# Optimization experiments

Measured on AMD Instinct MI355X. Metric: run time of the kernel, lower is better.

Reference implementation:

```python
import jax, jax.numpy as jnp
import numpy as np

N_NODES = 100000
N_EDGES = 1600000
N_ROOTS = 2048


def _with_self_loops(edge_index, num_nodes):
    loop = jnp.arange(num_nodes, dtype=edge_index.dtype)
    src = jnp.concatenate([edge_index[0], loop])
    dst = jnp.concatenate([edge_index[1], loop])
    return src, dst


def gcn_conv(x, w, b, src, dst, num_nodes):
    xw = x @ w  # [N, Fout]
    deg = jax.ops.segment_sum(jnp.ones_like(dst, dtype=xw.dtype), dst,
                              num_segments=num_nodes)
    dinv = jnp.where(deg > 0, jax.lax.rsqrt(jnp.maximum(deg, 1.0)) * (deg > 0), 0.0)
    dinv = jnp.where(deg > 0, deg ** -0.5, 0.0)
    norm = dinv[src] * dinv[dst]  # [E+N]
    msgs = norm[:, None] * xw[src]  # [E+N, Fout] -- dominant memory traffic
    out = jax.ops.segment_sum(msgs, dst, num_segments=num_nodes)
    return out + b


def setup_inputs() -> dict:
    key = jax.random.key(0)
    ks = jax.random.split(key, 10)
    x = jax.random.normal(ks[0], (N_NODES, 256), dtype=jnp.float32)
    edge_index = jax.random.randint(ks[1], (2, N_EDGES), 0, N_NODES, dtype=jnp.int32)
    bu_edge_index = jax.random.randint(ks[2], (2, N_EDGES), 0, N_NODES, dtype=jnp.int32)
    rootindex = jax.random.randint(ks[3], (N_ROOTS,), 0, N_NODES, dtype=jnp.int32)
    def glorot(k, shape):
        lim = (6.0 / (shape[0] + shape[1])) ** 0.5
        return jax.random.uniform(k, shape, jnp.float32, -lim, lim)
    return {
        "x": x, "edge_index": edge_index, "bu_edge_index": bu_edge_index,
        "rootindex": rootindex,
        "w1": glorot(ks[4], (256, 128)), "b1": jnp.zeros((128,), jnp.float32),
        "w2": glorot(ks[5], (128, 128)), "b2": jnp.zeros((128,), jnp.float32),
        "w3": glorot(ks[6], (256, 128)), "b3": jnp.zeros((128,), jnp.float32),
        "w4": glorot(ks[7], (128, 128)), "b4": jnp.zeros((128,), jnp.float32),
        "fc_w": glorot(ks[8], (256, 4)), "fc_b": jnp.zeros((4,), jnp.float32),
    }


def reference(x, edge_index, bu_edge_index, rootindex,
              w1, b1, w2, b2, w3, b3, w4, b4, fc_w, fc_b):
    n = x.shape[0]
    src_td, dst_td = _with_self_loops(edge_index, n)
    src_bu, dst_bu = _with_self_loops(bu_edge_index, n)

    # Top-down branch (dropout is identity in eval mode)
    h = jax.nn.elu(gcn_conv(x, w1, b1, src_td, dst_td, n))
    h = jax.nn.elu(gcn_conv(h, w2, b2, src_td, dst_td, n))
    h = h[rootindex]  # [B, 128]

    # Bottom-up branch
    h1 = jax.nn.elu(gcn_conv(x, w3, b3, src_bu, dst_bu, n))
    h1 = jax.nn.elu(gcn_conv(h1, w4, b4, src_bu, dst_bu, n))
    h1 = h1[rootindex]  # [B, 128]

    feat = jnp.concatenate([h, h1], axis=1)  # [B, 256]
    logits = feat @ fc_w + fc_b  # [B, 4]
    return jax.nn.log_softmax(logits, axis=1)
```

## Files before the change

kernel.cpp:

```cpp
#include <hip/hip_runtime.h>
#include <hip/hip_fp16.h>
#include <math.h>

typedef __attribute__((ext_vector_type(8))) short short8v;
typedef __attribute__((ext_vector_type(4))) float float4v;
typedef __attribute__((ext_vector_type(8))) unsigned short ushort8v;

#define CH 4096
#define MAXNB 800

#define SWZ(row, ck) ((ck) ^ (((row) >> 1) & 3))

__device__ inline unsigned short f2bf(float f) {
    unsigned u = __float_as_uint(f);
    return (unsigned short)((u + 0x7FFFu + ((u >> 16) & 1u)) >> 16);
}


__global__ __launch_bounds__(256) void bin1_kernel(const int* __restrict__ dst, int E, int NB,
                                                   int* __restrict__ gcnt,
                                                   int* __restrict__ blockBase) {
    __shared__ int h[MAXNB];
    int t = threadIdx.x;
    for (int i = t; i < NB; i += 256) h[i] = 0;
    __syncthreads();
    int e0 = blockIdx.x * CH;
#pragma unroll
    for (int i = 0; i < CH / 256; ++i) {
        int e = e0 + t + i * 256;
        if (e < E) atomicAdd(&h[dst[e] >> 7], 1);
    }
    __syncthreads();
    for (int b = t; b < NB; b += 256) {
        int c = h[b];
        int old = atomicAdd(&gcnt[b], c);
        blockBase[(size_t)blockIdx.x * MAXNB + b] = old;
    }
}


__global__ void scan1_kernel(const int* __restrict__ cnt, int N,
                             int* __restrict__ offs) {
    __shared__ int sd[256];
    int t = threadIdx.x;
    int base = t * 4;
    int v[4]; int s = 0;
#pragma unroll
    for (int i = 0; i < 4; ++i) { v[i] = (base + i < N) ? cnt[base + i] : 0; s += v[i]; }
    sd[t] = s; __syncthreads();
    for (int d = 1; d < 256; d <<= 1) {
        int x = (t >= d) ? sd[t - d] : 0;
        __syncthreads();
        sd[t] += x;
        __syncthreads();
    }
    int p = sd[t] - s;
#pragma unroll
    for (int i = 0; i < 4; ++i) { if (base + i < N) offs[base + i] = p; p += v[i]; }
}


__global__ __launch_bounds__(256) void bin2_kernel(const int* __restrict__ src,
                                                   const int* __restrict__ dst, int E, int NB,
                                                   const int* __restrict__ boff,
                                                   const int* __restrict__ blockBase,
                                                   int* __restrict__ ebuf) {
    __shared__ int h[MAXNB];
    __shared__ int intra[MAXNB];
    __shared__ int cursor[MAXNB];
    __shared__ int gbase[MAXNB];
    __shared__ int ps[256];
    __shared__ int sorted[CH];
    int t = threadIdx.x;
    int blk = blockIdx.x;
    for (int i = t; i < NB; i += 256) h[i] = 0;
    __syncthreads();
    int e0 = blk * CH;
#pragma unroll
    for (int i = 0; i < CH / 256; ++i) {
        int e = e0 + t + i * 256;
        if (e < E) atomicAdd(&h[dst[e] >> 7], 1);
    }
    __syncthreads();
    int base4 = t * 4;
    int v[4]; int s = 0;
#pragma unroll
    for (int k = 0; k < 4; ++k) { v[k] = (base4 + k < NB) ? h[base4 + k] : 0; s += v[k]; }
    ps[t] = s; __syncthreads();
    for (int d = 1; d < 256; d <<= 1) {
        int x = (t >= d) ? ps[t - d] : 0;
        __syncthreads();
        ps[t] += x;
        __syncthreads();
    }
    int p = ps[t] - s;
#pragma unroll
    for (int k = 0; k < 4; ++k) { if (base4 + k < NB) intra[base4 + k] = p; p += v[k]; }
    __syncthreads();
    for (int b = t; b < NB; b += 256) {
        cursor[b] = intra[b];
        gbase[b] = boff[b] + blockBase[(size_t)blk * MAXNB + b] - intra[b];
    }
    __syncthreads();
#pragma unroll
    for (int i = 0; i < CH / 256; ++i) {
        int e = e0 + t + i * 256;
        if (e < E) {
            int d = dst[e];
            int b = d >> 7;
            int pos = atomicAdd(&cursor[b], 1);
            sorted[pos] = (src[e] << 7) | (d & 127);
        }
    }
    __syncthreads();
    int lim = E - e0; if (lim > CH) lim = CH;
    for (int i = t; i < lim; i += 256) {
        int pr = sorted[i];
        int lo = 0, hi = NB - 1;
        while (lo < hi) {
            int mid = (lo + hi + 1) >> 1;
            if (intra[mid] <= i) lo = mid; else hi = mid - 1;
        }
        ebuf[(size_t)gbase[lo] + i] = pr;
    }
}


__global__ __launch_bounds__(256) void csr_build_kernel(const int* __restrict__ ebuf,
                                                        const int* __restrict__ boff,
                                                        const int* __restrict__ gcnt,
                                                        int* __restrict__ csr,
                                                        int* __restrict__ offs,
                                                        int* __restrict__ cnt,
                                                        float* __restrict__ dinv, int N) {
    __shared__ int h[128];
    __shared__ int sc[128];
    __shared__ int loc[128];
    __shared__ int cur[128];
    int t = threadIdx.x, b = blockIdx.x;
    if (t < 128) h[t] = 0;
    __syncthreads();
    int o = boff[b], c = gcnt[b];
    for (int i = t; i < c; i += 256) atomicAdd(&h[ebuf[o + i] & 127], 1);
    __syncthreads();
    if (t < 128) sc[t] = h[t];
    __syncthreads();
    for (int d = 1; d < 128; d <<= 1) {
        int x = (t >= d && t < 128) ? sc[t - d] : 0;
        __syncthreads();
        if (t < 128) sc[t] += x;
        __syncthreads();
    }
    if (t < 128) { loc[t] = sc[t] - h[t]; cur[t] = loc[t]; }
    __syncthreads();
    for (int i = t; i < c; i += 256) {
        int pr = ebuf[o + i];
        int pos = atomicAdd(&cur[pr & 127], 1);
        csr[o + pos] = pr >> 7;
    }
    if (t < 128) {
        int v = b * 128 + t;
        if (v < N) {
            offs[v] = o + loc[t];
            cnt[v] = h[t];
            dinv[v] = rsqrtf((float)(h[t] + 1));
        }
    }
}


__global__ __launch_bounds__(256) void mark_kernel(const int* __restrict__ roots, int R,
                                                   const int* __restrict__ csr,
                                                   const int* __restrict__ offs,
                                                   const int* __restrict__ cnt,
                                                   unsigned char* __restrict__ flag) {
    int wid = (blockIdx.x * blockDim.x + threadIdx.x) >> 6;
    if (wid >= R) return;
    int lane = threadIdx.x & 63;
    int r = roots[wid];
    int o = offs[r], c = cnt[r];
    for (int i = lane; i < c; i += 64) flag[csr[o + i]] = 1;
    if (lane == 0) flag[r] = 1;
}

__global__ __launch_bounds__(256) void compact_kernel(const unsigned char* __restrict__ flag,
                                                      int N, int* __restrict__ nlist,
                                                      int* __restrict__ list,
                                                      int* __restrict__ inv) {
    int v = blockIdx.x * blockDim.x + threadIdx.x;
    if (v < N && flag[v]) {
        int p = atomicAdd(nlist, 1);
        list[p] = v;
        inv[v] = p;
    }
}


__global__ void wsplit_kernel(const float* __restrict__ W, int K,
                              unsigned short* __restrict__ WThi,
                              unsigned short* __restrict__ WTlo) {
    int i = blockIdx.x * blockDim.x + threadIdx.x;
    if (i >= K * 128) return;
    int k = i >> 7, c = i & 127;
    float w = W[i];
    unsigned short hh = f2bf(w);
    float hf = __uint_as_float((unsigned)hh << 16);
    WThi[(size_t)c * K + k] = hh;
    WTlo[(size_t)c * K + k] = f2bf(w - hf);
}


__global__ __launch_bounds__(256) void gemm1_dual_kernel(const float* __restrict__ A,
                                                         const unsigned short* __restrict__ Bhi0,
                                                         const unsigned short* __restrict__ Blo0,
                                                         const unsigned short* __restrict__ Bhi1,
                                                         const unsigned short* __restrict__ Blo1,
                                                         __half* __restrict__ C0,
                                                         __half* __restrict__ C1,
                                                         int M, int K) {
    __shared__ unsigned short Ah[128 * 32];
    __shared__ unsigned short Al[128 * 32];
    __shared__ unsigned short Bh[2][128 * 32];
    __shared__ unsigned short Bl[2][128 * 32];
    int t = threadIdx.x;
    int w = t >> 6, l = t & 63;
    int lr = l & 15, lk = l >> 4;
    int row0 = blockIdx.x * 128;

    float4v acc[2][2][8];
#pragma unroll
    for (int b = 0; b < 2; ++b)
#pragma unroll
        for (int mf = 0; mf < 2; ++mf)
#pragma unroll
            for (int nf = 0; nf < 8; ++nf) acc[b][mf][nf] = (float4v){0.f, 0.f, 0.f, 0.f};

    for (int k0 = 0; k0 < K; k0 += 32) {
#pragma unroll
        for (int i = 0; i < 2; ++i) {
            int idx = t + i * 256;
            int r = idx >> 2, ck = idx & 3;
            int gr = row0 + r;
            float4 v0 = {0.f, 0.f, 0.f, 0.f}, v1 = {0.f, 0.f, 0.f, 0.f};
            if (gr < M) {
                const float* p = A + (size_t)gr * K + k0 + ck * 8;
                v0 = *(const float4*)p;
                v1 = *(const float4*)(p + 4);
            }
            float fs[8] = {v0.x, v0.y, v0.z, v0.w, v1.x, v1.y, v1.z, v1.w};
            ushort8v hi, lo;
#pragma unroll
            for (int j = 0; j < 8; ++j) {
                unsigned short hh = f2bf(fs[j]);
                hi[j] = hh;
                lo[j] = f2bf(fs[j] - __uint_as_float((unsigned)hh << 16));
            }
            int pos = r * 32 + SWZ(r, ck) * 8;
            *(ushort8v*)&Ah[pos] = hi;
            *(ushort8v*)&Al[pos] = lo;
        }
#pragma unroll
        for (int i = 0; i < 2; ++i) {
            int idx = t + i * 256;
            int col = idx >> 2, ck = idx & 3;
            size_t g = (size_t)col * K + k0 + ck * 8;
            int pos = col * 32 + SWZ(col, ck) * 8;
            *(ushort8v*)&Bh[0][pos] = *(const ushort8v*)(Bhi0 + g);
            *(ushort8v*)&Bl[0][pos] = *(const ushort8v*)(Blo0 + g);
            *(ushort8v*)&Bh[1][pos] = *(const ushort8v*)(Bhi1 + g);
            *(ushort8v*)&Bl[1][pos] = *(const ushort8v*)(Blo1 + g);
        }
        __syncthreads();

        int ar0 = w * 32 + lr, ar1 = w * 32 + 16 + lr;
        short8v ah0 = *(const short8v*)&Ah[ar0 * 32 + SWZ(ar0, lk) * 8];
        short8v al0 = *(const short8v*)&Al[ar0 * 32 + SWZ(ar0, lk) * 8];
        short8v ah1 = *(const short8v*)&Ah[ar1 * 32 + SWZ(ar1, lk) * 8];
        short8v al1 = *(const short8v*)&Al[ar1 * 32 + SWZ(ar1, lk) * 8];
#pragma unroll
        for (int nf = 0; nf < 8; ++nf) {
            int brow = nf * 16 + lr;
            int bpos = brow * 32 + SWZ(brow, lk) * 8;
            short8v bh0 = *(const short8v*)&Bh[0][bpos];
            short8v bl0 = *(const short8v*)&Bl[0][bpos];
            acc[0][0][nf] = __builtin_amdgcn_mfma_f32_16x16x32_bf16(ah0, bh0, acc[0][0][nf], 0, 0, 0);
            acc[0][0][nf] = __builtin_amdgcn_mfma_f32_16x16x32_bf16(ah0, bl0, acc[0][0][nf], 0, 0, 0);
            acc[0][0][nf] = __builtin_amdgcn_mfma_f32_16x16x32_bf16(al0, bh0, acc[0][0][nf], 0, 0, 0);
            acc[0][1][nf] = __builtin_amdgcn_mfma_f32_16x16x32_bf16(ah1, bh0, acc[0][1][nf], 0, 0, 0);
            acc[0][1][nf] = __builtin_amdgcn_mfma_f32_16x16x32_bf16(ah1, bl0, acc[0][1][nf], 0, 0, 0);
            acc[0][1][nf] = __builtin_amdgcn_mfma_f32_16x16x32_bf16(al1, bh0, acc[0][1][nf], 0, 0, 0);
            short8v bh1 = *(const short8v*)&Bh[1][bpos];
            short8v bl1 = *(const short8v*)&Bl[1][bpos];
            acc[1][0][nf] = __builtin_amdgcn_mfma_f32_16x16x32_bf16(ah0, bh1, acc[1][0][nf], 0, 0, 0);
            acc[1][0][nf] = __builtin_amdgcn_mfma_f32_16x16x32_bf16(ah0, bl1, acc[1][0][nf], 0, 0, 0);
            acc[1][0][nf] = __builtin_amdgcn_mfma_f32_16x16x32_bf16(al0, bh1, acc[1][0][nf], 0, 0, 0);
            acc[1][1][nf] = __builtin_amdgcn_mfma_f32_16x16x32_bf16(ah1, bh1, acc[1][1][nf], 0, 0, 0);
            acc[1][1][nf] = __builtin_amdgcn_mfma_f32_16x16x32_bf16(ah1, bl1, acc[1][1][nf], 0, 0, 0);
            acc[1][1][nf] = __builtin_amdgcn_mfma_f32_16x16x32_bf16(al1, bh1, acc[1][1][nf], 0, 0, 0);
        }
        __syncthreads();
    }
#pragma unroll
    for (int mf = 0; mf < 2; ++mf)
#pragma unroll
        for (int nf = 0; nf < 8; ++nf)
#pragma unroll
            for (int r = 0; r < 4; ++r) {
                int grow = row0 + w * 32 + mf * 16 + lk * 4 + r;
                if (grow < M) {
                    C0[(size_t)grow * 128 + nf * 16 + lr] = __float2half(acc[0][mf][nf][r]);
                    C1[(size_t)grow * 128 + nf * 16 + lr] = __float2half(acc[1][mf][nf][r]);
                }
            }
}


__global__ __launch_bounds__(256) void gemm_mfma_kernel(const float* __restrict__ A,
                                                        const unsigned short* __restrict__ WThi,
                                                        const unsigned short* __restrict__ WTlo,
                                                        __half* __restrict__ C, int M,
                                                        const int* __restrict__ Mdev, int K) {
    if (Mdev) M = *Mdev;
    int row0 = blockIdx.x * 128;
    if (row0 >= M) return;
    __shared__ unsigned short Ah[128 * 32];
    __shared__ unsigned short Al[128 * 32];
    __shared__ unsigned short Bh[128 * 32];
    __shared__ unsigned short Bl[128 * 32];
    int t = threadIdx.x;
    int w = t >> 6, l = t & 63;
    int lr = l & 15, lk = l >> 4;

    float4v acc[2][8];
#pragma unroll
    for (int mf = 0; mf < 2; ++mf)
#pragma unroll
        for (int nf = 0; nf < 8; ++nf) acc[mf][nf] = (float4v){0.f, 0.f, 0.f, 0.f};

    for (int k0 = 0; k0 < K; k0 += 32) {
#pragma unroll
        for (int i = 0; i < 2; ++i) {
            int idx = t + i * 256;
            int r = idx >> 2, ck = idx & 3;
            int gr = row0 + r;
            float4 v0 = {0.f, 0.f, 0.f, 0.f}, v1 = {0.f, 0.f, 0.f, 0.f};
            if (gr < M) {
                const float* p = A + (size_t)gr * K + k0 + ck * 8;
                v0 = *(const float4*)p;
                v1 = *(const float4*)(p + 4);
            }
            float fs[8] = {v0.x, v0.y, v0.z, v0.w, v1.x, v1.y, v1.z, v1.w};
            ushort8v hi, lo;
#pragma unroll
            for (int j = 0; j < 8; ++j) {
                unsigned short hh = f2bf(fs[j]);
                hi[j] = hh;
                lo[j] = f2bf(fs[j] - __uint_as_float((unsigned)hh << 16));
            }
            int pos = r * 32 + SWZ(r, ck) * 8;
            *(ushort8v*)&Ah[pos] = hi;
            *(ushort8v*)&Al[pos] = lo;
        }
#pragma unroll
        for (int i = 0; i < 2; ++i) {
            int idx = t + i * 256;
            int col = idx >> 2, ck = idx & 3;
            size_t g = (size_t)col * K + k0 + ck * 8;
            int pos = col * 32 + SWZ(col, ck) * 8;
            *(ushort8v*)&Bh[pos] = *(const ushort8v*)(WThi + g);
            *(ushort8v*)&Bl[pos] = *(const ushort8v*)(WTlo + g);
        }
        __syncthreads();

        int ar0 = w * 32 + lr, ar1 = w * 32 + 16 + lr;
        short8v ah0 = *(const short8v*)&Ah[ar0 * 32 + SWZ(ar0, lk) * 8];
        short8v al0 = *(const short8v*)&Al[ar0 * 32 + SWZ(ar0, lk) * 8];
        short8v ah1 = *(const short8v*)&Ah[ar1 * 32 + SWZ(ar1, lk) * 8];
        short8v al1 = *(const short8v*)&Al[ar1 * 32 + SWZ(ar1, lk) * 8];
#pragma unroll
        for (int nf = 0; nf < 8; ++nf) {
            int brow = nf * 16 + lr;
            int bpos = brow * 32 + SWZ(brow, lk) * 8;
            short8v bh = *(const short8v*)&Bh[bpos];
            short8v bl = *(const short8v*)&Bl[bpos];
            acc[0][nf] = __builtin_amdgcn_mfma_f32_16x16x32_bf16(ah0, bh, acc[0][nf], 0, 0, 0);
            acc[0][nf] = __builtin_amdgcn_mfma_f32_16x16x32_bf16(ah0, bl, acc[0][nf], 0, 0, 0);
            acc[0][nf] = __builtin_amdgcn_mfma_f32_16x16x32_bf16(al0, bh, acc[0][nf], 0, 0, 0);
            acc[1][nf] = __builtin_amdgcn_mfma_f32_16x16x32_bf16(ah1, bh, acc[1][nf], 0, 0, 0);
            acc[1][nf] = __builtin_amdgcn_mfma_f32_16x16x32_bf16(ah1, bl, acc[1][nf], 0, 0, 0);
            acc[1][nf] = __builtin_amdgcn_mfma_f32_16x16x32_bf16(al1, bh, acc[1][nf], 0, 0, 0);
        }
        __syncthreads();
    }
#pragma unroll
    for (int mf = 0; mf < 2; ++mf)
#pragma unroll
        for (int nf = 0; nf < 8; ++nf)
#pragma unroll
            for (int r = 0; r < 4; ++r) {
                int grow = row0 + w * 32 + mf * 16 + lk * 4 + r;
                if (grow < M) C[(size_t)grow * 128 + nf * 16 + lr] = __float2half(acc[mf][nf][r]);
            }
}


__global__ __launch_bounds__(256) void agg_kernel(const __half* __restrict__ xw,
                                                  const int* __restrict__ csr,
                                                  const int* __restrict__ offs,
                                                  const int* __restrict__ cnt,
                                                  const float* __restrict__ dinv,
                                                  const float* __restrict__ bias,
                                                  const int* __restrict__ nodelist,
                                                  const int* __restrict__ nwork_dev, int nwork,
                                                  float* __restrict__ out) {
    if (nwork_dev) nwork = *nwork_dev;
    int wid = (blockIdx.x * blockDim.x + threadIdx.x) >> 6;
    if (wid >= nwork) return;
    int lane = threadIdx.x & 63;
    int v = nodelist ? nodelist[wid] : wid;
    int o = offs[v];
    int c = cnt[v];
    float dv = dinv[v];
    float ax = 0.f, ay = 0.f;

    for (int base = 0; base < c; base += 64) {
        int rem = c - base; if (rem > 64) rem = 64;
        int li = base + lane; if (li >= c) li = c - 1;
        int s_l = csr[o + li];
        float d_l = dinv[s_l];
        int j = 0;
        for (; j + 4 <= rem; j += 4) {
            int s0 = __shfl(s_l, j);     int s1 = __shfl(s_l, j + 1);
            int s2 = __shfl(s_l, j + 2); int s3 = __shfl(s_l, j + 3);
            float e0 = __shfl(d_l, j);     float e1 = __shfl(d_l, j + 1);
            float e2 = __shfl(d_l, j + 2); float e3 = __shfl(d_l, j + 3);
            float2 v0 = __half22float2(*(const __half2*)(xw + (size_t)s0 * 128 + lane * 2));
            float2 v1 = __half22float2(*(const __half2*)(xw + (size_t)s1 * 128 + lane * 2));
            float2 v2 = __half22float2(*(const __half2*)(xw + (size_t)s2 * 128 + lane * 2));
            float2 v3 = __half22float2(*(const __half2*)(xw + (size_t)s3 * 128 + lane * 2));
            ax += e0 * v0.x + e1 * v1.x + e2 * v2.x + e3 * v3.x;
            ay += e0 * v0.y + e1 * v1.y + e2 * v2.y + e3 * v3.y;
        }
        for (; j < rem; ++j) {
            int s = __shfl(s_l, j);
            float e = __shfl(d_l, j);
            float2 vv = __half22float2(*(const __half2*)(xw + (size_t)s * 128 + lane * 2));
            ax += e * vv.x; ay += e * vv.y;
        }
    }
    float2 sv = __half22float2(*(const __half2*)(xw + (size_t)v * 128 + lane * 2));
    ax += dv * sv.x; ay += dv * sv.y;
    ax = dv * ax + bias[lane * 2];
    ay = dv * ay + bias[lane * 2 + 1];
    ax = ax > 0.f ? ax : expm1f(ax);
    ay = ay > 0.f ? ay : expm1f(ay);
    float2 res = {ax, ay};
    *(float2*)(out + (size_t)wid * 128 + lane * 2) = res;
}


__global__ __launch_bounds__(256) void root_agg_kernel(const __half* __restrict__ xwc,
                                                       const int* __restrict__ inv,
                                                       const int* __restrict__ csr,
                                                       const int* __restrict__ offs,
                                                       const int* __restrict__ cnt,
                                                       const float* __restrict__ dinv,
                                                       const float* __restrict__ bias,
                                                       const int* __restrict__ roots, int R,
                                                       float* __restrict__ feat, int col0) {
    int wid = (blockIdx.x * blockDim.x + threadIdx.x) >> 6;
    if (wid >= R) return;
    int lane = threadIdx.x & 63;
    int r = roots[wid];
    int o = offs[r], c = cnt[r];
    float dv = dinv[r];
    float ax = 0.f, ay = 0.f;
    for (int base = 0; base < c; base += 64) {
        int rem = c - base; if (rem > 64) rem = 64;
        int li = base + lane; if (li >= c) li = c - 1;
        int s_l = csr[o + li];
        float d_l = dinv[s_l];
        int iv_l = inv[s_l];
        for (int j = 0; j < rem; ++j) {
            int iv = __shfl(iv_l, j);
            float e = __shfl(d_l, j);
            float2 vv = __half22float2(*(const __half2*)(xwc + (size_t)iv * 128 + lane * 2));
            ax += e * vv.x; ay += e * vv.y;
        }
    }
    int ivr = inv[r];
    float2 sv = __half22float2(*(const __half2*)(xwc + (size_t)ivr * 128 + lane * 2));
    ax += dv * sv.x; ay += dv * sv.y;
    ax = dv * ax + bias[lane * 2];
    ay = dv * ay + bias[lane * 2 + 1];
    ax = ax > 0.f ? ax : expm1f(ax);
    ay = ay > 0.f ? ay : expm1f(ay);
    float2 res = {ax, ay};
    *(float2*)(feat + (size_t)wid * 256 + col0 + lane * 2) = res;
}


__global__ __launch_bounds__(256) void head_kernel(const float* __restrict__ feat,
                                                   const float* __restrict__ fcw,
                                                   const float* __restrict__ fcb,
                                                   float* __restrict__ out, int R) {
    int wid = (blockIdx.x * blockDim.x + threadIdx.x) >> 6;
    if (wid >= R) return;
    int lane = threadIdx.x & 63;
    const float* fr = feat + (size_t)wid * 256;
    float a0 = 0.f, a1 = 0.f, a2 = 0.f, a3 = 0.f;
    for (int k = lane; k < 256; k += 64) {
        float f = fr[k];
        float4 w = *(const float4*)(fcw + k * 4);
        a0 += f * w.x; a1 += f * w.y; a2 += f * w.z; a3 += f * w.w;
    }
#pragma unroll
    for (int d = 1; d < 64; d <<= 1) {
        a0 += __shfl_xor(a0, d); a1 += __shfl_xor(a1, d);
        a2 += __shfl_xor(a2, d); a3 += __shfl_xor(a3, d);
    }
    if (lane == 0) {
        a0 += fcb[0]; a1 += fcb[1]; a2 += fcb[2]; a3 += fcb[3];
        float m = fmaxf(fmaxf(a0, a1), fmaxf(a2, a3));
        float s = expf(a0 - m) + expf(a1 - m) + expf(a2 - m) + expf(a3 - m);
        float ls = logf(s) + m;
        float4 rr = {a0 - ls, a1 - ls, a2 - ls, a3 - ls};
        *(float4*)(out + (size_t)wid * 4) = rr;
    }
}


extern "C" void kernel_launch(void* const* d_in, const int* in_sizes, int n_in,
                              void* d_out, int out_size, void* d_ws, size_t ws_size,
                              hipStream_t stream) {
    const float* x    = (const float*)d_in[0];
    const int*   ei   = (const int*)d_in[1];
    const int*   bei  = (const int*)d_in[2];
    const int*   roots= (const int*)d_in[3];
    const float* w1 = (const float*)d_in[4];
    const float* b1 = (const float*)d_in[5];
    const float* w2 = (const float*)d_in[6];
    const float* b2 = (const float*)d_in[7];
    const float* w3 = (const float*)d_in[8];
    const float* b3 = (const float*)d_in[9];
    const float* w4 = (const float*)d_in[10];
    const float* b4 = (const float*)d_in[11];
    const float* fcw = (const float*)d_in[12];
    const float* fcb = (const float*)d_in[13];
    float* out = (float*)d_out;

    const int N = in_sizes[0] / 256;
    const int E = in_sizes[1] / 2;
    const int R = in_sizes[3];
    const int NB = (N + 127) >> 7;
    const int nblk = (E + CH - 1) / CH;

    char* ws = (char*)d_ws;
    size_t off = 0;
    auto alloc = [&](size_t b) { size_t o = off; off += (b + 255) & ~(size_t)255; return o; };
    __half* xw0   = (__half*)(ws + alloc((size_t)N * 128 * 2));
    __half* xw1   = (__half*)(ws + alloc((size_t)N * 128 * 2));
    __half* xw2c  = (__half*)(ws + alloc((size_t)N * 128 * 2));
    float*  hc    = (float*)(ws + alloc((size_t)N * 128 * 4));
    int*   ebuf = (int*)(ws + alloc((size_t)E * 4));
    int*   blockBase = (int*)(ws + alloc((size_t)nblk * MAXNB * 4));
    int*   gcnt = (int*)(ws + alloc((size_t)MAXNB * 4));
    int*   boff = (int*)(ws + alloc((size_t)MAXNB * 4));
    int*   csrA[2]; int* offsA[2]; int* cntA[2]; float* dinvA[2];
    int*   listA[2]; int* invA[2]; int* nlistA[2];
    unsigned char* flagA[2];
    for (int br = 0; br < 2; ++br) {
        csrA[br]  = (int*)(ws + alloc((size_t)E * 4));
        offsA[br] = (int*)(ws + alloc((size_t)N * 4));
        cntA[br]  = (int*)(ws + alloc((size_t)N * 4));
        dinvA[br] = (float*)(ws + alloc((size_t)N * 4));
        flagA[br] = (unsigned char*)(ws + alloc((size_t)N));
        listA[br] = (int*)(ws + alloc((size_t)N * 4));
        invA[br]  = (int*)(ws + alloc((size_t)N * 4));
        nlistA[br]= (int*)(ws + alloc(256));
    }
    float* feat = (float*)(ws + alloc((size_t)R * 256 * 4));
    unsigned short* WThi[4]; unsigned short* WTlo[4];
    for (int i = 0; i < 4; ++i) {
        int K = (i < 2) ? 256 : 128;
        WThi[i] = (unsigned short*)(ws + alloc((size_t)128 * K * 2));
        WTlo[i] = (unsigned short*)(ws + alloc((size_t)128 * K * 2));
    }

    for (int br = 0; br < 2; ++br) {
        const int* e    = (br == 0) ? ei : bei;
        const int* srcp = e;
        const int* dstp = e + E;
        hipMemsetAsync(gcnt, 0, (size_t)MAXNB * 4, stream);
        hipMemsetAsync(flagA[br], 0, (size_t)N, stream);
        hipMemsetAsync(nlistA[br], 0, 4, stream);
        bin1_kernel<<<nblk, 256, 0, stream>>>(dstp, E, NB, gcnt, blockBase);
        scan1_kernel<<<1, 256, 0, stream>>>(gcnt, NB, boff);
        bin2_kernel<<<nblk, 256, 0, stream>>>(srcp, dstp, E, NB, boff, blockBase, ebuf);
        csr_build_kernel<<<NB, 256, 0, stream>>>(ebuf, boff, gcnt, csrA[br], offsA[br],
                                                 cntA[br], dinvA[br], N);
        mark_kernel<<<(R * 64 + 255) / 256, 256, 0, stream>>>(roots, R, csrA[br], offsA[br],
                                                              cntA[br], flagA[br]);
        compact_kernel<<<(N + 255) / 256, 256, 0, stream>>>(flagA[br], N, nlistA[br],
                                                            listA[br], invA[br]);
    }

    wsplit_kernel<<<(256 * 128 + 255) / 256, 256, 0, stream>>>(w1, 256, WThi[0], WTlo[0]);
    wsplit_kernel<<<(256 * 128 + 255) / 256, 256, 0, stream>>>(w3, 256, WThi[1], WTlo[1]);
    wsplit_kernel<<<(128 * 128 + 255) / 256, 256, 0, stream>>>(w2, 128, WThi[2], WTlo[2]);
    wsplit_kernel<<<(128 * 128 + 255) / 256, 256, 0, stream>>>(w4, 128, WThi[3], WTlo[3]);

    gemm1_dual_kernel<<<(N + 127) / 128, 256, 0, stream>>>(
        x, WThi[0], WTlo[0], WThi[1], WTlo[1], xw0, xw1, N, 256);

    for (int br = 0; br < 2; ++br) {
        const __half* xwb = (br == 0) ? xw0 : xw1;
        const float* bA = (br == 0) ? b1 : b3;
        const float* bB = (br == 0) ? b2 : b4;
        agg_kernel<<<((size_t)N * 64 + 255) / 256, 256, 0, stream>>>(
            xwb, csrA[br], offsA[br], cntA[br], dinvA[br], bA, listA[br], nlistA[br], N, hc);
        gemm_mfma_kernel<<<(N + 127) / 128, 256, 0, stream>>>(
            hc, WThi[2 + br], WTlo[2 + br], xw2c, N, nlistA[br], 128);
        root_agg_kernel<<<((size_t)R * 64 + 255) / 256, 256, 0, stream>>>(
            xw2c, invA[br], csrA[br], offsA[br], cntA[br], dinvA[br], bB, roots, R,
            feat, br * 128);
    }
    head_kernel<<<((size_t)R * 64 + 255) / 256, 256, 0, stream>>>(feat, fcw, fcb, out, R);
}
```

Before: 558.3 us.

## Load GEMM operands directly from global memory and drop binary search in binning

Both MFMA GEMM kernels stop staging A and B tiles in shared memory. Each wave now loads its A fragment and the bf16 hi/lo weight fragments straight from global memory into registers, which removes the LDS writes, the swizzle and the per-k barriers, and adds launch bounds asking for two blocks per CU. The cost is redundant global and L2 reads of the weights across waves and less coalesced strided A loads. Separately, bin2 records each sorted entry's bucket id in shared memory so the scatter no longer binary-searches the prefix array.

```diff
diff --git a/kernel.cpp b/kernel.cpp
--- a/kernel.cpp
+++ b/kernel.cpp
@@ -9,11 +9,18 @@
 #define CH 4096
 #define MAXNB 800
 
-#define SWZ(row, ck) ((ck) ^ (((row) >> 1) & 3))
-
 __device__ inline unsigned short f2bf(float f) {
     unsigned u = __float_as_uint(f);
     return (unsigned short)((u + 0x7FFFu + ((u >> 16) & 1u)) >> 16);
+}
+
+__device__ inline void split8(const float* fs, short8v& hi, short8v& lo) {
+#pragma unroll
+    for (int j = 0; j < 8; ++j) {
+        unsigned short hh = f2bf(fs[j]);
+        hi[j] = (short)hh;
+        lo[j] = (short)f2bf(fs[j] - __uint_as_float((unsigned)hh << 16));
+    }
 }
 
 
@@ -71,6 +78,7 @@
     __shared__ int gbase[MAXNB];
     __shared__ int ps[256];
     __shared__ int sorted[CH];
+    __shared__ unsigned short sb[CH];
     int t = threadIdx.x;
     int blk = blockIdx.x;
     for (int i = t; i < NB; i += 256) h[i] = 0;
@@ -110,18 +118,13 @@
             int b = d >> 7;
             int pos = atomicAdd(&cursor[b], 1);
             sorted[pos] = (src[e] << 7) | (d & 127);
+            sb[pos] = (unsigned short)b;
         }
     }
     __syncthreads();
     int lim = E - e0; if (lim > CH) lim = CH;
     for (int i = t; i < lim; i += 256) {
-        int pr = sorted[i];
-        int lo = 0, hi = NB - 1;
-        while (lo < hi) {
-            int mid = (lo + hi + 1) >> 1;
-            if (intra[mid] <= i) lo = mid; else hi = mid - 1;
-        }
-        ebuf[(size_t)gbase[lo] + i] = pr;
+        ebuf[(size_t)gbase[sb[i]] + i] = sorted[i];
     }
 }
 
@@ -210,22 +213,23 @@
 }
 
 
-__global__ __launch_bounds__(256) void gemm1_dual_kernel(const float* __restrict__ A,
-                                                         const unsigned short* __restrict__ Bhi0,
-                                                         const unsigned short* __restrict__ Blo0,
-                                                         const unsigned short* __restrict__ Bhi1,
-                                                         const unsigned short* __restrict__ Blo1,
-                                                         __half* __restrict__ C0,
-                                                         __half* __restrict__ C1,
-                                                         int M, int K) {
-    __shared__ unsigned short Ah[128 * 32];
-    __shared__ unsigned short Al[128 * 32];
-    __shared__ unsigned short Bh[2][128 * 32];
-    __shared__ unsigned short Bl[2][128 * 32];
+__global__ __launch_bounds__(256, 2) void gemm1_dual_kernel(const float* __restrict__ A,
+                                                            const unsigned short* __restrict__ Bhi0,
+                                                            const unsigned short* __restrict__ Blo0,
+                                                            const unsigned short* __restrict__ Bhi1,
+                                                            const unsigned short* __restrict__ Blo1,
+                                                            __half* __restrict__ C0,
+                                                            __half* __restrict__ C1,
+                                                            int M, int K) {
     int t = threadIdx.x;
     int w = t >> 6, l = t & 63;
     int lr = l & 15, lk = l >> 4;
-    int row0 = blockIdx.x * 128;
+    int rowbase = blockIdx.x * 128 + w * 32;
+    int r0 = rowbase + lr, r1 = rowbase + 16 + lr;
+    int r0c = r0 < M ? r0 : M - 1;
+    int r1c = r1 < M ? r1 : M - 1;
+    const float* a0p = A + (size_t)r0c * K + lk * 8;
+    const float* a1p = A + (size_t)r1c * K + lk * 8;
 
     float4v acc[2][2][8];
 #pragma unroll
@@ -235,62 +239,30 @@
 #pragma unroll
             for (int nf = 0; nf < 8; ++nf) acc[b][mf][nf] = (float4v){0.f, 0.f, 0.f, 0.f};
 
+#pragma unroll 2
     for (int k0 = 0; k0 < K; k0 += 32) {
-#pragma unroll
-        for (int i = 0; i < 2; ++i) {
-            int idx = t + i * 256;
-            int r = idx >> 2, ck = idx & 3;
-            int gr = row0 + r;
-            float4 v0 = {0.f, 0.f, 0.f, 0.f}, v1 = {0.f, 0.f, 0.f, 0.f};
-            if (gr < M) {
-                const float* p = A + (size_t)gr * K + k0 + ck * 8;
-                v0 = *(const float4*)p;
-                v1 = *(const float4*)(p + 4);
-            }
-            float fs[8] = {v0.x, v0.y, v0.z, v0.w, v1.x, v1.y, v1.z, v1.w};
-            ushort8v hi, lo;
-#pragma unroll
-            for (int j = 0; j < 8; ++j) {
-                unsigned short hh = f2bf(fs[j]);
-                hi[j] = hh;
-                lo[j] = f2bf(fs[j] - __uint_as_float((unsigned)hh << 16));
-            }
-            int pos = r * 32 + SWZ(r, ck) * 8;
-            *(ushort8v*)&Ah[pos] = hi;
-            *(ushort8v*)&Al[pos] = lo;
-        }
-#pragma unroll
-        for (int i = 0; i < 2; ++i) {
-            int idx = t + i * 256;
-            int col = idx >> 2, ck = idx & 3;
-            size_t g = (size_t)col * K + k0 + ck * 8;
-            int pos = col * 32 + SWZ(col, ck) * 8;
-            *(ushort8v*)&Bh[0][pos] = *(const ushort8v*)(Bhi0 + g);
-            *(ushort8v*)&Bl[0][pos] = *(const ushort8v*)(Blo0 + g);
-            *(ushort8v*)&Bh[1][pos] = *(const ushort8v*)(Bhi1 + g);
-            *(ushort8v*)&Bl[1][pos] = *(const ushort8v*)(Blo1 + g);
-        }
-        __syncthreads();
-
-        int ar0 = w * 32 + lr, ar1 = w * 32 + 16 + lr;
-        short8v ah0 = *(const short8v*)&Ah[ar0 * 32 + SWZ(ar0, lk) * 8];
-        short8v al0 = *(const short8v*)&Al[ar0 * 32 + SWZ(ar0, lk) * 8];
-        short8v ah1 = *(const short8v*)&Ah[ar1 * 32 + SWZ(ar1, lk) * 8];
-        short8v al1 = *(const short8v*)&Al[ar1 * 32 + SWZ(ar1, lk) * 8];
+        float fs0[8], fs1[8];
+        *(float4*)&fs0[0] = *(const float4*)(a0p + k0);
+        *(float4*)&fs0[4] = *(const float4*)(a0p + k0 + 4);
+        *(float4*)&fs1[0] = *(const float4*)(a1p + k0);
+        *(float4*)&fs1[4] = *(const float4*)(a1p + k0 + 4);
+        short8v ah0, al0, ah1, al1;
+        split8(fs0, ah0, al0);
+        split8(fs1, ah1, al1);
+        size_t bo = (size_t)lr * K + k0 + lk * 8;
 #pragma unroll
         for (int nf = 0; nf < 8; ++nf) {
-            int brow = nf * 16 + lr;
-            int bpos = brow * 32 + SWZ(brow, lk) * 8;
-            short8v bh0 = *(const short8v*)&Bh[0][bpos];
-            short8v bl0 = *(const short8v*)&Bl[0][bpos];
+            size_t g = bo + (size_t)nf * 16 * K;
+            short8v bh0 = *(const short8v*)(Bhi0 + g);
+            short8v bl0 = *(const short8v*)(Blo0 + g);
             acc[0][0][nf] = __builtin_amdgcn_mfma_f32_16x16x32_bf16(ah0, bh0, acc[0][0][nf], 0, 0, 0);
             acc[0][0][nf] = __builtin_amdgcn_mfma_f32_16x16x32_bf16(ah0, bl0, acc[0][0][nf], 0, 0, 0);
             acc[0][0][nf] = __builtin_amdgcn_mfma_f32_16x16x32_bf16(al0, bh0, acc[0][0][nf], 0, 0, 0);
             acc[0][1][nf] = __builtin_amdgcn_mfma_f32_16x16x32_bf16(ah1, bh0, acc[0][1][nf], 0, 0, 0);
             acc[0][1][nf] = __builtin_amdgcn_mfma_f32_16x16x32_bf16(ah1, bl0, acc[0][1][nf], 0, 0, 0);
             acc[0][1][nf] = __builtin_amdgcn_mfma_f32_16x16x32_bf16(al1, bh0, acc[0][1][nf], 0, 0, 0);
-            short8v bh1 = *(const short8v*)&Bh[1][bpos];
-            short8v bl1 = *(const short8v*)&Bl[1][bpos];
+            short8v bh1 = *(const short8v*)(Bhi1 + g);
+            short8v bl1 = *(const short8v*)(Blo1 + g);
             acc[1][0][nf] = __builtin_amdgcn_mfma_f32_16x16x32_bf16(ah0, bh1, acc[1][0][nf], 0, 0, 0);
             acc[1][0][nf] = __builtin_amdgcn_mfma_f32_16x16x32_bf16(ah0, bl1, acc[1][0][nf], 0, 0, 0);
             acc[1][0][nf] = __builtin_amdgcn_mfma_f32_16x16x32_bf16(al0, bh1, acc[1][0][nf], 0, 0, 0);
@@ -298,7 +270,6 @@
             acc[1][1][nf] = __builtin_amdgcn_mfma_f32_16x16x32_bf16(ah1, bl1, acc[1][1][nf], 0, 0, 0);
             acc[1][1][nf] = __builtin_amdgcn_mfma_f32_16x16x32_bf16(al1, bh1, acc[1][1][nf], 0, 0, 0);
         }
-        __syncthreads();
     }
 #pragma unroll
     for (int mf = 0; mf < 2; ++mf)
@@ -306,7 +277,7 @@
         for (int nf = 0; nf < 8; ++nf)
 #pragma unroll
             for (int r = 0; r < 4; ++r) {
-                int grow = row0 + w * 32 + mf * 16 + lk * 4 + r;
+                int grow = rowbase + mf * 16 + lk * 4 + r;
                 if (grow < M) {
                     C0[(size_t)grow * 128 + nf * 16 + lr] = __float2half(acc[0][mf][nf][r]);
                     C1[(size_t)grow * 128 + nf * 16 + lr] = __float2half(acc[1][mf][nf][r]);
@@ -315,21 +286,22 @@
 }
 
 
-__global__ __launch_bounds__(256) void gemm_mfma_kernel(const float* __restrict__ A,
-                                                        const unsigned short* __restrict__ WThi,
-                                                        const unsigned short* __restrict__ WTlo,
-                                                        __half* __restrict__ C, int M,
-                                                        const int* __restrict__ Mdev, int K) {
+__global__ __launch_bounds__(256, 2) void gemm_mfma_kernel(const float* __restrict__ A,
+                                                           const unsigned short* __restrict__ WThi,
+                                                           const unsigned short* __restrict__ WTlo,
+                                                           __half* __restrict__ C, int M,
+                                                           const int* __restrict__ Mdev, int K) {
     if (Mdev) M = *Mdev;
-    int row0 = blockIdx.x * 128;
-    if (row0 >= M) return;
-    __shared__ unsigned short Ah[128 * 32];
-    __shared__ unsigned short Al[128 * 32];
-    __shared__ unsigned short Bh[128 * 32];
-    __shared__ unsigned short Bl[128 * 32];
     int t = threadIdx.x;
     int w = t >> 6, l = t & 63;
     int lr = l & 15, lk = l >> 4;
+    int rowbase = blockIdx.x * 128 + w * 32;
+    if (rowbase >= M) return;
+    int r0 = rowbase + lr, r1 = rowbase + 16 + lr;
+    int r0c = r0 < M ? r0 : M - 1;
+    int r1c = r1 < M ? r1 : M - 1;
+    const float* a0p = A + (size_t)r0c * K + lk * 8;
+    const float* a1p = A + (size_t)r1c * K + lk * 8;
 
     float4v acc[2][8];
 #pragma unroll
@@ -337,52 +309,22 @@
 #pragma unroll
         for (int nf = 0; nf < 8; ++nf) acc[mf][nf] = (float4v){0.f, 0.f, 0.f, 0.f};
 
+#pragma unroll 2
     for (int k0 = 0; k0 < K; k0 += 32) {
-#pragma unroll
-        for (int i = 0; i < 2; ++i) {
-            int idx = t + i * 256;
-            int r = idx >> 2, ck = idx & 3;
-            int gr = row0 + r;
-            float4 v0 = {0.f, 0.f, 0.f, 0.f}, v1 = {0.f, 0.f, 0.f, 0.f};
-            if (gr < M) {
-                const float* p = A + (size_t)gr * K + k0 + ck * 8;
-                v0 = *(const float4*)p;
-                v1 = *(const float4*)(p + 4);
-            }
-            float fs[8] = {v0.x, v0.y, v0.z, v0.w, v1.x, v1.y, v1.z, v1.w};
-            ushort8v hi, lo;
-#pragma unroll
-            for (int j = 0; j < 8; ++j) {
-                unsigned short hh = f2bf(fs[j]);
-                hi[j] = hh;
-                lo[j] = f2bf(fs[j] - __uint_as_float((unsigned)hh << 16));
-            }
-            int pos = r * 32 + SWZ(r, ck) * 8;
-            *(ushort8v*)&Ah[pos] = hi;
-            *(ushort8v*)&Al[pos] = lo;
-        }
-#pragma unroll
-        for (int i = 0; i < 2; ++i) {
-            int idx = t + i * 256;
-            int col = idx >> 2, ck = idx & 3;
-            size_t g = (size_t)col * K + k0 + ck * 8;
-            int pos = col * 32 + SWZ(col, ck) * 8;
-            *(ushort8v*)&Bh[pos] = *(const ushort8v*)(WThi + g);
-            *(ushort8v*)&Bl[pos] = *(const ushort8v*)(WTlo + g);
-        }
-        __syncthreads();
-
-        int ar0 = w * 32 + lr, ar1 = w * 32 + 16 + lr;
-        short8v ah0 = *(const short8v*)&Ah[ar0 * 32 + SWZ(ar0, lk) * 8];
-        short8v al0 = *(const short8v*)&Al[ar0 * 32 + SWZ(ar0, lk) * 8];
-        short8v ah1 = *(const short8v*)&Ah[ar1 * 32 + SWZ(ar1, lk) * 8];
-        short8v al1 = *(const short8v*)&Al[ar1 * 32 + SWZ(ar1, lk) * 8];
+        float fs0[8], fs1[8];
+        *(float4*)&fs0[0] = *(const float4*)(a0p + k0);
+        *(float4*)&fs0[4] = *(const float4*)(a0p + k0 + 4);
+        *(float4*)&fs1[0] = *(const float4*)(a1p + k0);
+        *(float4*)&fs1[4] = *(const float4*)(a1p + k0 + 4);
+        short8v ah0, al0, ah1, al1;
+        split8(fs0, ah0, al0);
+        split8(fs1, ah1, al1);
+        size_t bo = (size_t)lr * K + k0 + lk * 8;
 #pragma unroll
         for (int nf = 0; nf < 8; ++nf) {
-            int brow = nf * 16 + lr;
-            int bpos = brow * 32 + SWZ(brow, lk) * 8;
-            short8v bh = *(const short8v*)&Bh[bpos];
-            short8v bl = *(const short8v*)&Bl[bpos];
+            size_t g = bo + (size_t)nf * 16 * K;
+            short8v bh = *(const short8v*)(WThi + g);
+            short8v bl = *(const short8v*)(WTlo + g);
             acc[0][nf] = __builtin_amdgcn_mfma_f32_16x16x32_bf16(ah0, bh, acc[0][nf], 0, 0, 0);
             acc[0][nf] = __builtin_amdgcn_mfma_f32_16x16x32_bf16(ah0, bl, acc[0][nf], 0, 0, 0);
             acc[0][nf] = __builtin_amdgcn_mfma_f32_16x16x32_bf16(al0, bh, acc[0][nf], 0, 0, 0);
@@ -390,7 +332,6 @@
             acc[1][nf] = __builtin_amdgcn_mfma_f32_16x16x32_bf16(ah1, bl, acc[1][nf], 0, 0, 0);
             acc[1][nf] = __builtin_amdgcn_mfma_f32_16x16x32_bf16(al1, bh, acc[1][nf], 0, 0, 0);
         }
-        __syncthreads();
     }
 #pragma unroll
     for (int mf = 0; mf < 2; ++mf)
@@ -398,7 +339,7 @@
         for (int nf = 0; nf < 8; ++nf)
 #pragma unroll
             for (int r = 0; r < 4; ++r) {
-                int grow = row0 + w * 32 + mf * 16 + lk * 4 + r;
+                int grow = rowbase + mf * 16 + lk * 4 + r;
                 if (grow < M) C[(size_t)grow * 128 + nf * 16 + lr] = __float2half(acc[mf][nf][r]);
             }
 }
```

New measurement: 600.3 us. 7.5% more time.
